# Kernel optimization log

Measured on AMD Instinct MI355X. Metric: run time of the kernel, lower is better.

## Reference

```python
import jax, jax.numpy as jnp
import numpy as np

N = 50000      # nodes
E = 800000     # edges
F_IN = 128     # input_channels
H = 128        # hidden_channels
OUT = 10       # output_channels
G = 64         # graphs in batch


def setup_inputs() -> dict:
    key = jax.random.key(0)
    ks = jax.random.split(key, 16)
    s = 0.05
    inp = {
        "x": jax.random.normal(ks[0], (N, F_IN), jnp.float32),
        "edge_index": jax.random.randint(ks[1], (2, E), 0, N, jnp.int64 if jax.config.jax_enable_x64 else jnp.int32),
        "batch": jnp.sort(jax.random.randint(ks[2], (N,), 0, G, jnp.int32)),
        "conv1_w": jax.random.normal(ks[3], (F_IN, H), jnp.float32) * s,
        "conv1_b": jnp.zeros((H,), jnp.float32),
        "conv2_w": jax.random.normal(ks[4], (H, H), jnp.float32) * s,
        "conv2_b": jnp.zeros((H,), jnp.float32),
        "conv3_w": jax.random.normal(ks[5], (H, H), jnp.float32) * s,
        "conv3_b": jnp.zeros((H,), jnp.float32),
        "fc1_w": jax.random.normal(ks[6], (H, 8 * H), jnp.float32) * s,
        "fc1_b": jnp.zeros((8 * H,), jnp.float32),
        "fc2_w": jax.random.normal(ks[7], (8 * H, 4 * H), jnp.float32) * s,
        "fc2_b": jnp.zeros((4 * H,), jnp.float32),
        "fc3_w": jax.random.normal(ks[8], (4 * H, 2 * H), jnp.float32) * s,
        "fc3_b": jnp.zeros((2 * H,), jnp.float32),
        "fc4_w": jax.random.normal(ks[9], (2 * H, H), jnp.float32) * s,
        "fc4_b": jnp.zeros((H,), jnp.float32),
        "fc5_w": jax.random.normal(ks[10], (H, OUT), jnp.float32) * s,
        "fc5_b": jnp.zeros((OUT,), jnp.float32),
    }
    return inp


def _gcn_conv(x, w, b, src, dst, norm, n_nodes):
    # GCNConv: out = D^{-1/2} (A + I) D^{-1/2} X W + b   (self-loops already in src/dst)
    xw = x @ w                                        # [N, H]
    msg = xw[src] * norm[:, None]                     # gather + scale, [E+N, H]
    return jax.ops.segment_sum(msg, dst, num_segments=n_nodes) + b


def reference(x, edge_index, batch,
              conv1_w, conv1_b, conv2_w, conv2_b, conv3_w, conv3_b,
              fc1_w, fc1_b, fc2_w, fc2_b, fc3_w, fc3_b,
              fc4_w, fc4_b, fc5_w, fc5_b):
    n = x.shape[0]
    loop = jnp.arange(n, dtype=edge_index.dtype)
    src = jnp.concatenate([edge_index[0], loop])      # add self-loops
    dst = jnp.concatenate([edge_index[1], loop])
    deg = jax.ops.segment_sum(jnp.ones_like(dst, dtype=x.dtype), dst, num_segments=n)
    dinv = jnp.where(deg > 0, jax.lax.rsqrt(deg), 0.0)
    norm = dinv[src] * dinv[dst]                      # symmetric normalization per edge

    h = jax.nn.relu(_gcn_conv(x, conv1_w, conv1_b, src, dst, norm, n))
    h = jax.nn.relu(_gcn_conv(h, conv2_w, conv2_b, src, dst, norm, n))
    h = _gcn_conv(h, conv3_w, conv3_b, src, dst, norm, n)

    # global mean pool over graphs
    sums = jax.ops.segment_sum(h, batch, num_segments=G)
    cnt = jax.ops.segment_sum(jnp.ones((n,), x.dtype), batch, num_segments=G)
    f = sums / jnp.maximum(cnt, 1.0)[:, None]         # [G, H]

    y = jax.nn.relu(f @ fc1_w + fc1_b)
    y = jax.nn.relu(y @ fc2_w + fc2_b)
    y = jax.nn.relu(y @ fc3_w + fc3_b)
    y = jax.nn.relu(y @ fc4_w + fc4_b)
    # dropout p=0.5 is identity in eval mode
    y = y @ fc5_w + fc5_b                             # [G, OUT]
    return (f, y)
```

## Files before the change

### kernel.cpp

```cpp
#include <hip/hip_runtime.h>
#include <stdint.h>

#define N_NODES 50000
#define N_EDGES 800000
#define FEAT    128
#define NGRAPH  64

#define XB_BLKS   6250
#define W_BLKS    32
#define E_BLKS    3125
#define PREP_BLKS (XB_BLKS + W_BLKS + E_BLKS)
#define GEMM_BLKS 6250

typedef __attribute__((ext_vector_type(8))) short short8;
typedef __attribute__((ext_vector_type(4))) float floatx4;

static __device__ __forceinline__ ushort f2bf(float f) {
  uint32_t x = __float_as_uint(f);
  x += 0x7FFF + ((x >> 16) & 1);
  return (ushort)(x >> 16);
}
static __device__ __forceinline__ float bfLo(uint32_t u) {
  return __uint_as_float(u << 16);
}
static __device__ __forceinline__ float bfHi(uint32_t u) {
  return __uint_as_float(u & 0xFFFF0000u);
}

static __device__ __forceinline__ void cvt4(const float* __restrict__ in,
                                            ushort* __restrict__ out, int i) {
  float4 v = ((const float4*)in)[i];
  ushort4 u;
  u.x = f2bf(v.x); u.y = f2bf(v.y); u.z = f2bf(v.z); u.w = f2bf(v.w);
  ((ushort4*)out)[i] = u;
}

static __device__ __forceinline__ void cvt4T(const float* __restrict__ in,
                                             ushort* __restrict__ outT, int i) {
  float4 v = ((const float4*)in)[i];
  int k = (4 * i) >> 7;
  int n = (4 * i) & 127;
  outT[(size_t)(n + 0) * FEAT + k] = f2bf(v.x);
  outT[(size_t)(n + 1) * FEAT + k] = f2bf(v.y);
  outT[(size_t)(n + 2) * FEAT + k] = f2bf(v.z);
  outT[(size_t)(n + 3) * FEAT + k] = f2bf(v.w);
}

__global__ __launch_bounds__(256) void prep_fused(const float* __restrict__ x,
                                                  ushort* __restrict__ xb,
                                                  const float* __restrict__ w0,
                                                  const float* __restrict__ w1,
                                                  ushort* __restrict__ wbT,
                                                  const int* __restrict__ dst,
                                                  int* __restrict__ cnt,
                                                  int* __restrict__ rank) {
  int b = blockIdx.x, t = threadIdx.x;
  if (b < XB_BLKS) {
    cvt4(x, xb, b * 256 + t);
  } else if (b < XB_BLKS + W_BLKS) {
    int i = (b - XB_BLKS) * 256 + t;
    if (i < 4096) cvt4T(w0, wbT, i);
    else cvt4T(w1, wbT + FEAT * FEAT, i - 4096);
  } else {
    int e = (b - XB_BLKS - W_BLKS) * 256 + t;
    if (e < N_EDGES) rank[e] = atomicAdd(&cnt[dst[e]], 1);
  }
}

__global__ __launch_bounds__(256) void dinv_scan1(const int* __restrict__ cnt,
                                                  const int* __restrict__ batch,
                                                  float* __restrict__ dinv,
                                                  float* __restrict__ cnt_g,
                                                  int* __restrict__ ptr,
                                                  int* __restrict__ bsums) {
  __shared__ int tmp[256];
  __shared__ int bins[NGRAPH];
  if (threadIdx.x < NGRAPH) bins[threadIdx.x] = 0;
  int i = blockIdx.x * 256 + threadIdx.x;
  int v = (i < N_NODES) ? cnt[i] : 0;
  tmp[threadIdx.x] = v;
  __syncthreads();
  for (int off = 1; off < 256; off <<= 1) {
    int t = (threadIdx.x >= off) ? tmp[threadIdx.x - off] : 0;
    __syncthreads();
    tmp[threadIdx.x] += t;
    __syncthreads();
  }
  if (i < N_NODES) ptr[i] = tmp[threadIdx.x] - v;
  if (threadIdx.x == 255) bsums[blockIdx.x] = tmp[255];
  if (i < N_NODES) {
    dinv[i] = rsqrtf((float)v + 1.0f);
    atomicAdd(&bins[batch[i]], 1);
  }
  __syncthreads();
  if (threadIdx.x < NGRAPH && bins[threadIdx.x] > 0)
    atomicAdd(&cnt_g[threadIdx.x], (float)bins[threadIdx.x]);
}

__global__ __launch_bounds__(256) void scan2(int* __restrict__ bsums, int nb) {
  __shared__ int tmp[256];
  int v = (threadIdx.x < nb) ? bsums[threadIdx.x] : 0;
  tmp[threadIdx.x] = v;
  __syncthreads();
  for (int off = 1; off < 256; off <<= 1) {
    int t = (threadIdx.x >= off) ? tmp[threadIdx.x - off] : 0;
    __syncthreads();
    tmp[threadIdx.x] += t;
    __syncthreads();
  }
  if (threadIdx.x < nb) bsums[threadIdx.x] = tmp[threadIdx.x] - v;
}

__global__ __launch_bounds__(256) void scan3(int* __restrict__ ptr,
                                             const int* __restrict__ bsums) {
  int i = blockIdx.x * 256 + threadIdx.x;
  if (i < N_NODES) ptr[i] += bsums[blockIdx.x];
}

static __device__ __forceinline__ void gemm_body(int wave, int lane,
                                                 const ushort* __restrict__ X,
                                                 const ushort* __restrict__ WT,
                                                 ushort* __restrict__ XW,
                                                 const float* __restrict__ dinv) {
  int mt = wave >> 3;
  int nt = wave & 7;
  if (mt >= N_NODES / 16) return;
  int m0 = mt * 16, n0 = nt * 16;
  int r = lane & 15, quad = lane >> 4;
  floatx4 acc = {0.f, 0.f, 0.f, 0.f};
  const ushort* xrow = X + (size_t)(m0 + r) * FEAT;
  const ushort* wrow = WT + (size_t)(n0 + r) * FEAT;
#pragma unroll
  for (int kb = 0; kb < 4; ++kb) {
    int k0 = kb * 32 + quad * 8;
    short8 a = *(const short8*)(xrow + k0);
    short8 b = *(const short8*)(wrow + k0);
    acc = __builtin_amdgcn_mfma_f32_16x16x32_bf16(a, b, acc, 0, 0, 0);
  }
#pragma unroll
  for (int reg = 0; reg < 4; ++reg) {
    int row = quad * 4 + reg;
    float di = dinv[m0 + row];
    XW[(size_t)(m0 + row) * FEAT + n0 + r] = f2bf(acc[reg] * di);
  }
}

__global__ __launch_bounds__(256) void gemm128(const ushort* __restrict__ X,
                                               const ushort* __restrict__ WT,
                                               ushort* __restrict__ XW,
                                               const float* __restrict__ dinv) {
  gemm_body((blockIdx.x * 256 + threadIdx.x) >> 6, threadIdx.x & 63, X, WT, XW, dinv);
}

__global__ __launch_bounds__(256) void fill_gemm1(const ushort* __restrict__ X,
                                                  const ushort* __restrict__ WT,
                                                  ushort* __restrict__ XW,
                                                  const float* __restrict__ dinv,
                                                  const int* __restrict__ src,
                                                  const int* __restrict__ dst,
                                                  const int* __restrict__ ptr,
                                                  const int* __restrict__ rank,
                                                  int* __restrict__ esrc) {
  if (blockIdx.x < GEMM_BLKS) {
    gemm_body((blockIdx.x * 256 + threadIdx.x) >> 6, threadIdx.x & 63, X, WT, XW, dinv);
  } else {
    int e = (blockIdx.x - GEMM_BLKS) * 256 + threadIdx.x;
    if (e >= N_EDGES) return;
    esrc[ptr[dst[e]] + rank[e]] = src[e];
  }
}

template <int MODE>
__global__ __launch_bounds__(256) void agg_kernel(const ushort* __restrict__ msg,
                                                  const float* __restrict__ dinv,
                                                  const int* __restrict__ ptr,
                                                  const int* __restrict__ cnt,
                                                  const int* __restrict__ esrc,
                                                  const float* __restrict__ bias,
                                                  void* __restrict__ outp) {
  int wave = (blockIdx.x * 256 + threadIdx.x) >> 6;
  int lane = threadIdx.x & 63;
  if (wave >= N_NODES) return;
  int v = wave;
  float di = dinv[v];
  const uint32_t* m32 = (const uint32_t*)msg;
  uint32_t su = m32[(size_t)v * 64 + lane];
  float ax0 = bfLo(su), ay0 = bfHi(su);
  float ax1 = 0.f, ay1 = 0.f, ax2 = 0.f, ay2 = 0.f, ax3 = 0.f, ay3 = 0.f;
  int start = ptr[v];
  int n = cnt[v];
  int i = 0;
  int pre = (4 - (start & 3)) & 3;
  if (pre > n) pre = n;
  for (; i < pre; ++i) {
    uint32_t u = m32[(size_t)esrc[start + i] * 64 + lane];
    ax0 += bfLo(u); ay0 += bfHi(u);
  }
  for (; i + 8 <= n; i += 8) {
    const int4* ep = (const int4*)(esrc + start + i);
    int4 q0 = ep[0], q1 = ep[1];
    uint32_t u0 = m32[(size_t)q0.x * 64 + lane];
    uint32_t u1 = m32[(size_t)q0.y * 64 + lane];
    uint32_t u2 = m32[(size_t)q0.z * 64 + lane];
    uint32_t u3 = m32[(size_t)q0.w * 64 + lane];
    uint32_t u4 = m32[(size_t)q1.x * 64 + lane];
    uint32_t u5 = m32[(size_t)q1.y * 64 + lane];
    uint32_t u6 = m32[(size_t)q1.z * 64 + lane];
    uint32_t u7 = m32[(size_t)q1.w * 64 + lane];
    ax0 += bfLo(u0); ay0 += bfHi(u0);
    ax1 += bfLo(u1); ay1 += bfHi(u1);
    ax2 += bfLo(u2); ay2 += bfHi(u2);
    ax3 += bfLo(u3); ay3 += bfHi(u3);
    ax0 += bfLo(u4); ay0 += bfHi(u4);
    ax1 += bfLo(u5); ay1 += bfHi(u5);
    ax2 += bfLo(u6); ay2 += bfHi(u6);
    ax3 += bfLo(u7); ay3 += bfHi(u7);
  }
  for (; i < n; ++i) {
    uint32_t u = m32[(size_t)esrc[start + i] * 64 + lane];
    ax0 += bfLo(u); ay0 += bfHi(u);
  }
  float ax = (ax0 + ax1) + (ax2 + ax3);
  float ay = (ay0 + ay1) + (ay2 + ay3);
  if (MODE == 2) {
    ((float2*)outp)[(size_t)v * 64 + lane] = make_float2(ax * di, ay * di);
  } else {
    ax = fmaf(ax, di, bias[2 * lane]);
    ay = fmaf(ay, di, bias[2 * lane + 1]);
    ax = fmaxf(ax, 0.f);
    ay = fmaxf(ay, 0.f);
    if (MODE == 1) { ax *= di; ay *= di; }
    ushort2 h2;
    h2.x = f2bf(ax);
    h2.y = f2bf(ay);
    ((ushort2*)outp)[(size_t)v * 64 + lane] = h2;
  }
}

__global__ __launch_bounds__(256) void pool_sum(const float* __restrict__ a3,
                                                const int* __restrict__ batch,
                                                float* __restrict__ P) {
  int wave = blockIdx.x * 4 + (threadIdx.x >> 6);
  int lane = threadIdx.x & 63;
  int v0 = wave * 16;
  if (v0 >= N_NODES) return;
  int vend = v0 + 16;
  if (vend > N_NODES) vend = N_NODES;
  const float2* a2 = (const float2*)a3;
  float ax = 0.f, ay = 0.f;
  int g = batch[v0];
  for (int v = v0; v < vend; ++v) {
    int gv = batch[v];
    if (gv != g) {
      atomicAdd(&P[(size_t)g * FEAT + 2 * lane], ax);
      atomicAdd(&P[(size_t)g * FEAT + 2 * lane + 1], ay);
      ax = 0.f; ay = 0.f; g = gv;
    }
    float2 t = a2[(size_t)v * 64 + lane];
    ax += t.x;
    ay += t.y;
  }
  atomicAdd(&P[(size_t)g * FEAT + 2 * lane], ax);
  atomicAdd(&P[(size_t)g * FEAT + 2 * lane + 1], ay);
}

__device__ __forceinline__ void head_layer(const float* __restrict__ IN,
                                           float* __restrict__ OUT,
                                           const float* __restrict__ w,
                                           const float* __restrict__ b,
                                           int K, int C, int Cp, int relu,
                                           float* __restrict__ gout, int t) {
  int parts = 1024 / Cp;
  int part = t / Cp;
  int c = t - part * Cp;
  int kchunk = K / parts;
  if (t < C) OUT[t] = b[t];
  __syncthreads();
  if (c < C) {
    int k0 = part * kchunk;
    float a0 = 0.f, a1 = 0.f, a2 = 0.f, a3 = 0.f;
    const float* wp = w + (size_t)k0 * C + c;
    if ((kchunk & 3) == 0) {
#pragma unroll 4
      for (int k = 0; k < kchunk; k += 4) {
        a0 = fmaf(IN[k0 + k],     wp[(size_t)k * C],       a0);
        a1 = fmaf(IN[k0 + k + 1], wp[(size_t)(k + 1) * C], a1);
        a2 = fmaf(IN[k0 + k + 2], wp[(size_t)(k + 2) * C], a2);
        a3 = fmaf(IN[k0 + k + 3], wp[(size_t)(k + 3) * C], a3);
      }
    } else {
      for (int k = 0; k < kchunk; ++k)
        a0 = fmaf(IN[k0 + k], wp[(size_t)k * C], a0);
    }
    atomicAdd(&OUT[c], (a0 + a1) + (a2 + a3));
  }
  __syncthreads();
  if (t < C) {
    float v = OUT[t];
    if (relu) { v = fmaxf(v, 0.f); OUT[t] = v; }
    if (gout) gout[t] = v;
  }
  __syncthreads();
}

__global__ __launch_bounds__(1024) void fc_head(const float* __restrict__ P,
                                                const float* __restrict__ cnt_g,
                                                const float* __restrict__ w3,
                                                const float* __restrict__ b3,
                                                const float* __restrict__ w1,
                                                const float* __restrict__ b1,
                                                const float* __restrict__ w2,
                                                const float* __restrict__ b2,
                                                const float* __restrict__ wf3,
                                                const float* __restrict__ bf3,
                                                const float* __restrict__ w4,
                                                const float* __restrict__ b4,
                                                const float* __restrict__ w5,
                                                const float* __restrict__ b5,
                                                float* __restrict__ out_f,
                                                float* __restrict__ out_y) {
  __shared__ float A[1024];
  __shared__ float B[1024];
  int r = blockIdx.x, t = threadIdx.x;
  if (t < FEAT) A[t] = P[r * FEAT + t] / fmaxf(cnt_g[r], 1.0f);
  __syncthreads();
  head_layer(A, B, w3, b3, 128, 128, 128, 0, out_f + (size_t)r * FEAT, t);
  head_layer(B, A, w1, b1, 128, 1024, 1024, 1, nullptr, t);
  head_layer(A, B, w2, b2, 1024, 512, 512, 1, nullptr, t);
  head_layer(B, A, wf3, bf3, 512, 256, 256, 1, nullptr, t);
  head_layer(A, B, w4, b4, 256, 128, 128, 1, nullptr, t);
  head_layer(B, A, w5, b5, 128, 10, 16, 0, out_y + (size_t)r * 10, t);
}

extern "C" void kernel_launch(void* const* d_in, const int* in_sizes, int n_in,
                              void* d_out, int out_size, void* d_ws, size_t ws_size,
                              hipStream_t stream) {
  const float* x         = (const float*)d_in[0];
  const int*   ei        = (const int*)d_in[1];
  const int*   batch     = (const int*)d_in[2];
  const float* conv_w[3] = {(const float*)d_in[3], (const float*)d_in[5], (const float*)d_in[7]};
  const float* conv_b[3] = {(const float*)d_in[4], (const float*)d_in[6], (const float*)d_in[8]};
  const float* fc_w[5]   = {(const float*)d_in[9],  (const float*)d_in[11],
                            (const float*)d_in[13], (const float*)d_in[15],
                            (const float*)d_in[17]};
  const float* fc_b[5]   = {(const float*)d_in[10], (const float*)d_in[12],
                            (const float*)d_in[14], (const float*)d_in[16],
                            (const float*)d_in[18]};
  const int* e_src = ei;
  const int* e_dst = ei + N_EDGES;
  float* out_f = (float*)d_out;
  float* out_y = (float*)d_out + NGRAPH * FEAT;

  char* p = (char*)d_ws;
  auto carve = [&](size_t bytes) {
    char* r = p;
    p += (bytes + 255) & ~(size_t)255;
    return r;
  };
  int*    cnt_i   = (int*)carve(N_NODES * 4);
  float*  dinv    = (float*)carve(N_NODES * 4);
  int*    csr_ptr = (int*)carve(N_NODES * 4);
  int*    bsums   = (int*)carve(256 * 4);
  int*    rank    = (int*)carve((size_t)N_EDGES * 4);
  int*    esrc    = (int*)carve((size_t)N_EDGES * 4);
  ushort* xb      = (ushort*)carve((size_t)N_NODES * FEAT * 2);
  ushort* wbT     = (ushort*)carve((size_t)2 * FEAT * FEAT * 2);
  ushort* msl     = (ushort*)carve((size_t)N_NODES * FEAT * 2);
  ushort* hbuf    = (ushort*)carve((size_t)N_NODES * FEAT * 2);
  float*  f_sum   = (float*)carve(NGRAPH * FEAT * 4);
  float*  cnt_g   = (float*)carve(NGRAPH * 4);
  float* a3 = (float*)xb;

  const int BLK_N = (N_NODES + 255) / 256;

  hipMemsetAsync(cnt_i, 0, N_NODES * 4, stream);
  hipMemsetAsync(f_sum, 0, NGRAPH * FEAT * 4 + 256, stream);

  prep_fused<<<PREP_BLKS, 256, 0, stream>>>(x, xb, conv_w[0], conv_w[1], wbT,
                                            e_dst, cnt_i, rank);

  dinv_scan1<<<BLK_N, 256, 0, stream>>>(cnt_i, batch, dinv, cnt_g, csr_ptr, bsums);
  scan2<<<1, 256, 0, stream>>>(bsums, BLK_N);
  scan3<<<BLK_N, 256, 0, stream>>>(csr_ptr, bsums);

  fill_gemm1<<<GEMM_BLKS + E_BLKS, 256, 0, stream>>>(
      xb, wbT, msl, dinv, e_src, e_dst, csr_ptr, rank, esrc);

  const int AGG_BLKS  = (N_NODES + 3) / 4;
  const int POOL_BLKS = (N_NODES / 16 + 3) / 4 + 1;

  agg_kernel<0><<<AGG_BLKS, 256, 0, stream>>>(msl, dinv, csr_ptr, cnt_i, esrc,
                                              conv_b[0], hbuf);
  gemm128<<<GEMM_BLKS, 256, 0, stream>>>(hbuf, wbT + FEAT * FEAT, msl, dinv);
  agg_kernel<1><<<AGG_BLKS, 256, 0, stream>>>(msl, dinv, csr_ptr, cnt_i, esrc,
                                              conv_b[1], hbuf);
  agg_kernel<2><<<AGG_BLKS, 256, 0, stream>>>(hbuf, dinv, csr_ptr, cnt_i, esrc,
                                              nullptr, a3);
  pool_sum<<<POOL_BLKS, 256, 0, stream>>>(a3, batch, f_sum);

  fc_head<<<NGRAPH, 1024, 0, stream>>>(f_sum, cnt_g, conv_w[2], conv_b[2],
                                       fc_w[0], fc_b[0], fc_w[1], fc_b[1],
                                       fc_w[2], fc_b[2], fc_w[3], fc_b[3],
                                       fc_w[4], fc_b[4], out_f, out_y);
}
```

Baseline: 396.9 us.

## Fuse x bf16 conversion into first GEMM and store per-edge source norm in CSR

Removes the separate x-to-bf16 conversion pass: the first GEMM now reads fp32 x directly, converts it in registers, and is interleaved with the degree-count atomics. The CSR now stores (src, dinv[src]) pairs, so aggregation applies the source normalisation with an FMA instead of folding dinv into the GEMM outputs. Edge-list fill is split into its own kernel, and workspace buffers are aliased to cut memory footprint. This avoids one full read and write of the node features, but doubles the edge-list bytes read in each of the three aggregation passes.

```diff
diff --git a/kernel.cpp b/kernel.cpp
--- a/kernel.cpp
+++ b/kernel.cpp
@@ -6,11 +6,9 @@
 #define FEAT    128
 #define NGRAPH  64
 
-#define XB_BLKS   6250
-#define W_BLKS    32
 #define E_BLKS    3125
-#define PREP_BLKS (XB_BLKS + W_BLKS + E_BLKS)
 #define GEMM_BLKS 6250
+#define GR_BLKS   (GEMM_BLKS + E_BLKS)
 
 typedef __attribute__((ext_vector_type(8))) short short8;
 typedef __attribute__((ext_vector_type(4))) float floatx4;
@@ -25,14 +23,6 @@
 }
 static __device__ __forceinline__ float bfHi(uint32_t u) {
   return __uint_as_float(u & 0xFFFF0000u);
-}
-
-static __device__ __forceinline__ void cvt4(const float* __restrict__ in,
-                                            ushort* __restrict__ out, int i) {
-  float4 v = ((const float4*)in)[i];
-  ushort4 u;
-  u.x = f2bf(v.x); u.y = f2bf(v.y); u.z = f2bf(v.z); u.w = f2bf(v.w);
-  ((ushort4*)out)[i] = u;
 }
 
 static __device__ __forceinline__ void cvt4T(const float* __restrict__ in,
@@ -46,24 +36,60 @@
   outT[(size_t)(n + 3) * FEAT + k] = f2bf(v.w);
 }
 
-__global__ __launch_bounds__(256) void prep_fused(const float* __restrict__ x,
-                                                  ushort* __restrict__ xb,
-                                                  const float* __restrict__ w0,
-                                                  const float* __restrict__ w1,
-                                                  ushort* __restrict__ wbT,
-                                                  const int* __restrict__ dst,
-                                                  int* __restrict__ cnt,
-                                                  int* __restrict__ rank) {
+__global__ __launch_bounds__(256) void wcvt(const float* __restrict__ w0,
+                                            const float* __restrict__ w1,
+                                            ushort* __restrict__ wbT) {
+  int i = blockIdx.x * 256 + threadIdx.x;
+  if (i < 4096) cvt4T(w0, wbT, i);
+  else cvt4T(w1, wbT + FEAT * FEAT, i - 4096);
+}
+
+static __device__ __forceinline__ void gemm_body_f32a(int wave, int lane,
+                                                      const float* __restrict__ X,
+                                                      const ushort* __restrict__ WT,
+                                                      ushort* __restrict__ XW) {
+  int mt = wave >> 3;
+  int nt = wave & 7;
+  int m0 = mt * 16, n0 = nt * 16;
+  int r = lane & 15, quad = lane >> 4;
+  floatx4 acc = {0.f, 0.f, 0.f, 0.f};
+  const float* xrow = X + (size_t)(m0 + r) * FEAT;
+  const ushort* wrow = WT + (size_t)(n0 + r) * FEAT;
+#pragma unroll
+  for (int kb = 0; kb < 4; ++kb) {
+    int k0 = kb * 32 + quad * 8;
+    float4 f0 = *(const float4*)(xrow + k0);
+    float4 f1 = *(const float4*)(xrow + k0 + 4);
+    short8 a;
+    a[0] = (short)f2bf(f0.x); a[1] = (short)f2bf(f0.y);
+    a[2] = (short)f2bf(f0.z); a[3] = (short)f2bf(f0.w);
+    a[4] = (short)f2bf(f1.x); a[5] = (short)f2bf(f1.y);
+    a[6] = (short)f2bf(f1.z); a[7] = (short)f2bf(f1.w);
+    short8 b = *(const short8*)(wrow + k0);
+    acc = __builtin_amdgcn_mfma_f32_16x16x32_bf16(a, b, acc, 0, 0, 0);
+  }
+#pragma unroll
+  for (int reg = 0; reg < 4; ++reg) {
+    int row = quad * 4 + reg;
+    XW[(size_t)(m0 + row) * FEAT + n0 + r] = f2bf(acc[reg]);
+  }
+}
+
+__global__ __launch_bounds__(256) void gemm_rank(const float* __restrict__ x,
+                                                 const ushort* __restrict__ wbT,
+                                                 ushort* __restrict__ msl,
+                                                 const int* __restrict__ dst,
+                                                 int* __restrict__ cnt,
+                                                 int* __restrict__ rank) {
   int b = blockIdx.x, t = threadIdx.x;
-  if (b < XB_BLKS) {
-    cvt4(x, xb, b * 256 + t);
-  } else if (b < XB_BLKS + W_BLKS) {
-    int i = (b - XB_BLKS) * 256 + t;
-    if (i < 4096) cvt4T(w0, wbT, i);
-    else cvt4T(w1, wbT + FEAT * FEAT, i - 4096);
+  int third = b / 3;
+  int rem = b - third * 3;
+  if (rem < 2) {
+    int gb = third * 2 + rem;
+    gemm_body_f32a(gb * 4 + (t >> 6), t & 63, x, wbT, msl);
   } else {
-    int e = (b - XB_BLKS - W_BLKS) * 256 + t;
-    if (e < N_EDGES) rank[e] = atomicAdd(&cnt[dst[e]], 1);
+    int e = third * 256 + t;
+    rank[e] = atomicAdd(&cnt[dst[e]], 1);
   }
 }
 
@@ -117,14 +143,25 @@
   if (i < N_NODES) ptr[i] += bsums[blockIdx.x];
 }
 
-static __device__ __forceinline__ void gemm_body(int wave, int lane,
-                                                 const ushort* __restrict__ X,
-                                                 const ushort* __restrict__ WT,
-                                                 ushort* __restrict__ XW,
-                                                 const float* __restrict__ dinv) {
+__global__ __launch_bounds__(256) void fill_csr(const int* __restrict__ src,
+                                                const int* __restrict__ dst,
+                                                const int* __restrict__ rank,
+                                                const int* __restrict__ ptr,
+                                                const float* __restrict__ dinv,
+                                                int2* __restrict__ edges) {
+  int e = blockIdx.x * 256 + threadIdx.x;
+  if (e >= N_EDGES) return;
+  int s = src[e];
+  edges[ptr[dst[e]] + rank[e]] = make_int2(s, __float_as_int(dinv[s]));
+}
+
+__global__ __launch_bounds__(256) void gemm128(const ushort* __restrict__ X,
+                                               const ushort* __restrict__ WT,
+                                               ushort* __restrict__ XW) {
+  int wave = (blockIdx.x * 256 + threadIdx.x) >> 6;
+  int lane = threadIdx.x & 63;
   int mt = wave >> 3;
   int nt = wave & 7;
-  if (mt >= N_NODES / 16) return;
   int m0 = mt * 16, n0 = nt * 16;
   int r = lane & 15, quad = lane >> 4;
   floatx4 acc = {0.f, 0.f, 0.f, 0.f};
@@ -140,33 +177,7 @@
 #pragma unroll
   for (int reg = 0; reg < 4; ++reg) {
     int row = quad * 4 + reg;
-    float di = dinv[m0 + row];
-    XW[(size_t)(m0 + row) * FEAT + n0 + r] = f2bf(acc[reg] * di);
-  }
-}
-
-__global__ __launch_bounds__(256) void gemm128(const ushort* __restrict__ X,
-                                               const ushort* __restrict__ WT,
-                                               ushort* __restrict__ XW,
-                                               const float* __restrict__ dinv) {
-  gemm_body((blockIdx.x * 256 + threadIdx.x) >> 6, threadIdx.x & 63, X, WT, XW, dinv);
-}
-
-__global__ __launch_bounds__(256) void fill_gemm1(const ushort* __restrict__ X,
-                                                  const ushort* __restrict__ WT,
-                                                  ushort* __restrict__ XW,
-                                                  const float* __restrict__ dinv,
-                                                  const int* __restrict__ src,
-                                                  const int* __restrict__ dst,
-                                                  const int* __restrict__ ptr,
-                                                  const int* __restrict__ rank,
-                                                  int* __restrict__ esrc) {
-  if (blockIdx.x < GEMM_BLKS) {
-    gemm_body((blockIdx.x * 256 + threadIdx.x) >> 6, threadIdx.x & 63, X, WT, XW, dinv);
-  } else {
-    int e = (blockIdx.x - GEMM_BLKS) * 256 + threadIdx.x;
-    if (e >= N_EDGES) return;
-    esrc[ptr[dst[e]] + rank[e]] = src[e];
+    XW[(size_t)(m0 + row) * FEAT + n0 + r] = f2bf(acc[reg]);
   }
 }
 
@@ -175,7 +186,7 @@
                                                   const float* __restrict__ dinv,
                                                   const int* __restrict__ ptr,
                                                   const int* __restrict__ cnt,
-                                                  const int* __restrict__ esrc,
+                                                  const int2* __restrict__ edges,
                                                   const float* __restrict__ bias,
                                                   void* __restrict__ outp) {
   int wave = (blockIdx.x * 256 + threadIdx.x) >> 6;
@@ -185,40 +196,49 @@
   float di = dinv[v];
   const uint32_t* m32 = (const uint32_t*)msg;
   uint32_t su = m32[(size_t)v * 64 + lane];
-  float ax0 = bfLo(su), ay0 = bfHi(su);
+  float ax0 = di * bfLo(su), ay0 = di * bfHi(su);
   float ax1 = 0.f, ay1 = 0.f, ax2 = 0.f, ay2 = 0.f, ax3 = 0.f, ay3 = 0.f;
   int start = ptr[v];
   int n = cnt[v];
   int i = 0;
-  int pre = (4 - (start & 3)) & 3;
-  if (pre > n) pre = n;
-  for (; i < pre; ++i) {
-    uint32_t u = m32[(size_t)esrc[start + i] * 64 + lane];
-    ax0 += bfLo(u); ay0 += bfHi(u);
+  if ((start & 1) && n > 0) {
+    int2 e = edges[start];
+    uint32_t u = m32[(size_t)e.x * 64 + lane];
+    float nrm = __int_as_float(e.y);
+    ax0 = fmaf(nrm, bfLo(u), ax0);
+    ay0 = fmaf(nrm, bfHi(u), ay0);
+    i = 1;
   }
   for (; i + 8 <= n; i += 8) {
-    const int4* ep = (const int4*)(esrc + start + i);
-    int4 q0 = ep[0], q1 = ep[1];
+    const int4* ep = (const int4*)(edges + start + i);
+    int4 q0 = ep[0], q1 = ep[1], q2 = ep[2], q3 = ep[3];
     uint32_t u0 = m32[(size_t)q0.x * 64 + lane];
-    uint32_t u1 = m32[(size_t)q0.y * 64 + lane];
-    uint32_t u2 = m32[(size_t)q0.z * 64 + lane];
-    uint32_t u3 = m32[(size_t)q0.w * 64 + lane];
-    uint32_t u4 = m32[(size_t)q1.x * 64 + lane];
-    uint32_t u5 = m32[(size_t)q1.y * 64 + lane];
-    uint32_t u6 = m32[(size_t)q1.z * 64 + lane];
-    uint32_t u7 = m32[(size_t)q1.w * 64 + lane];
-    ax0 += bfLo(u0); ay0 += bfHi(u0);
-    ax1 += bfLo(u1); ay1 += bfHi(u1);
-    ax2 += bfLo(u2); ay2 += bfHi(u2);
-    ax3 += bfLo(u3); ay3 += bfHi(u3);
-    ax0 += bfLo(u4); ay0 += bfHi(u4);
-    ax1 += bfLo(u5); ay1 += bfHi(u5);
-    ax2 += bfLo(u6); ay2 += bfHi(u6);
-    ax3 += bfLo(u7); ay3 += bfHi(u7);
+    uint32_t u1 = m32[(size_t)q0.z * 64 + lane];
+    uint32_t u2 = m32[(size_t)q1.x * 64 + lane];
+    uint32_t u3 = m32[(size_t)q1.z * 64 + lane];
+    uint32_t u4 = m32[(size_t)q2.x * 64 + lane];
+    uint32_t u5 = m32[(size_t)q2.z * 64 + lane];
+    uint32_t u6 = m32[(size_t)q3.x * 64 + lane];
+    uint32_t u7 = m32[(size_t)q3.z * 64 + lane];
+    float n0 = __int_as_float(q0.y), n1 = __int_as_float(q0.w);
+    float n2 = __int_as_float(q1.y), n3 = __int_as_float(q1.w);
+    float n4 = __int_as_float(q2.y), n5 = __int_as_float(q2.w);
+    float n6 = __int_as_float(q3.y), n7 = __int_as_float(q3.w);
+    ax0 = fmaf(n0, bfLo(u0), ax0); ay0 = fmaf(n0, bfHi(u0), ay0);
+    ax1 = fmaf(n1, bfLo(u1), ax1); ay1 = fmaf(n1, bfHi(u1), ay1);
+    ax2 = fmaf(n2, bfLo(u2), ax2); ay2 = fmaf(n2, bfHi(u2), ay2);
+    ax3 = fmaf(n3, bfLo(u3), ax3); ay3 = fmaf(n3, bfHi(u3), ay3);
+    ax0 = fmaf(n4, bfLo(u4), ax0); ay0 = fmaf(n4, bfHi(u4), ay0);
+    ax1 = fmaf(n5, bfLo(u5), ax1); ay1 = fmaf(n5, bfHi(u5), ay1);
+    ax2 = fmaf(n6, bfLo(u6), ax2); ay2 = fmaf(n6, bfHi(u6), ay2);
+    ax3 = fmaf(n7, bfLo(u7), ax3); ay3 = fmaf(n7, bfHi(u7), ay3);
   }
   for (; i < n; ++i) {
-    uint32_t u = m32[(size_t)esrc[start + i] * 64 + lane];
-    ax0 += bfLo(u); ay0 += bfHi(u);
+    int2 e = edges[start + i];
+    float nrm = __int_as_float(e.y);
+    uint32_t u = m32[(size_t)e.x * 64 + lane];
+    ax0 = fmaf(nrm, bfLo(u), ax0);
+    ay0 = fmaf(nrm, bfHi(u), ay0);
   }
   float ax = (ax0 + ax1) + (ax2 + ax3);
   float ay = (ay0 + ay1) + (ay2 + ay3);
@@ -229,7 +249,6 @@
     ay = fmaf(ay, di, bias[2 * lane + 1]);
     ax = fmaxf(ax, 0.f);
     ay = fmaxf(ay, 0.f);
-    if (MODE == 1) { ax *= di; ay *= di; }
     ushort2 h2;
     h2.x = f2bf(ax);
     h2.y = f2bf(ay);
@@ -361,40 +380,40 @@
   float*  dinv    = (float*)carve(N_NODES * 4);
   int*    csr_ptr = (int*)carve(N_NODES * 4);
   int*    bsums   = (int*)carve(256 * 4);
-  int*    rank    = (int*)carve((size_t)N_EDGES * 4);
-  int*    esrc    = (int*)carve((size_t)N_EDGES * 4);
-  ushort* xb      = (ushort*)carve((size_t)N_NODES * FEAT * 2);
+  int2*   edges   = (int2*)carve((size_t)N_EDGES * 8);
   ushort* wbT     = (ushort*)carve((size_t)2 * FEAT * FEAT * 2);
-  ushort* msl     = (ushort*)carve((size_t)N_NODES * FEAT * 2);
   ushort* hbuf    = (ushort*)carve((size_t)N_NODES * FEAT * 2);
   float*  f_sum   = (float*)carve(NGRAPH * FEAT * 4);
   float*  cnt_g   = (float*)carve(NGRAPH * 4);
-  float* a3 = (float*)xb;
+  char*   region  = carve((size_t)N_NODES * FEAT * 4);
+  int*    rank    = (int*)region;
+  ushort* msl     = (ushort*)(region + (size_t)N_EDGES * 4);
+  float*  a3      = (float*)region;
 
   const int BLK_N = (N_NODES + 255) / 256;
 
   hipMemsetAsync(cnt_i, 0, N_NODES * 4, stream);
   hipMemsetAsync(f_sum, 0, NGRAPH * FEAT * 4 + 256, stream);
 
-  prep_fused<<<PREP_BLKS, 256, 0, stream>>>(x, xb, conv_w[0], conv_w[1], wbT,
-                                            e_dst, cnt_i, rank);
+  wcvt<<<32, 256, 0, stream>>>(conv_w[0], conv_w[1], wbT);
+
+  gemm_rank<<<GR_BLKS, 256, 0, stream>>>(x, wbT, msl, e_dst, cnt_i, rank);
 
   dinv_scan1<<<BLK_N, 256, 0, stream>>>(cnt_i, batch, dinv, cnt_g, csr_ptr, bsums);
   scan2<<<1, 256, 0, stream>>>(bsums, BLK_N);
   scan3<<<BLK_N, 256, 0, stream>>>(csr_ptr, bsums);
 
-  fill_gemm1<<<GEMM_BLKS + E_BLKS, 256, 0, stream>>>(
-      xb, wbT, msl, dinv, e_src, e_dst, csr_ptr, rank, esrc);
+  fill_csr<<<E_BLKS, 256, 0, stream>>>(e_src, e_dst, rank, csr_ptr, dinv, edges);
 
   const int AGG_BLKS  = (N_NODES + 3) / 4;
   const int POOL_BLKS = (N_NODES / 16 + 3) / 4 + 1;
 
-  agg_kernel<0><<<AGG_BLKS, 256, 0, stream>>>(msl, dinv, csr_ptr, cnt_i, esrc,
+  agg_kernel<0><<<AGG_BLKS, 256, 0, stream>>>(msl, dinv, csr_ptr, cnt_i, edges,
                                               conv_b[0], hbuf);
-  gemm128<<<GEMM_BLKS, 256, 0, stream>>>(hbuf, wbT + FEAT * FEAT, msl, dinv);
-  agg_kernel<1><<<AGG_BLKS, 256, 0, stream>>>(msl, dinv, csr_ptr, cnt_i, esrc,
+  gemm128<<<GEMM_BLKS, 256, 0, stream>>>(hbuf, wbT + FEAT * FEAT, msl);
+  agg_kernel<0><<<AGG_BLKS, 256, 0, stream>>>(msl, dinv, csr_ptr, cnt_i, edges,
                                               conv_b[1], hbuf);
-  agg_kernel<2><<<AGG_BLKS, 256, 0, stream>>>(hbuf, dinv, csr_ptr, cnt_i, esrc,
+  agg_kernel<2><<<AGG_BLKS, 256, 0, stream>>>(hbuf, dinv, csr_ptr, cnt_i, edges,
                                               nullptr, a3);
   pool_sum<<<POOL_BLKS, 256, 0, stream>>>(a3, batch, f_sum);
 
```

Result: faster. 373.5 us (-5.9%).
